# Optimization experiments

Hardware: AMD Instinct MI355X
Metric: run time of the kernel (lower is better)

The kernel has to match this reference:

```python
import jax, jax.numpy as jnp
import numpy as np

VOCAB = 32000
D_MODEL = 192
N_LAYERS = 8
D_STATE = 64
EXPAND = 2
D_CONV = 3
NUM_CLASSES = 2
D_INNER = EXPAND * D_MODEL            # 384
DT_RANK = (D_MODEL + 15) // 16        # 12 (mamba_ssm default ceil(d_model/16))
EPS = 1e-6


def rmsnorm(x, w):
    return w * x * jax.lax.rsqrt(jnp.mean(x * x, axis=-1, keepdims=True) + EPS)


def selective_scan(u, dt, A, Bm, Cm):
    # u, dt: (b, T, d_inner); Bm, Cm: (b, T, d_state); A: (d_inner, d_state)
    def step(h, xs):
        dt_t, B_t, C_t, u_t = xs                      # (b,di),(b,ds),(b,ds),(b,di)
        dA = jnp.exp(dt_t[:, :, None] * A)            # (b, di, ds)
        h = dA * h + (dt_t * u_t)[:, :, None] * B_t[:, None, :]
        y = jnp.einsum('bdn,bn->bd', h, C_t)
        return h, y

    b = u.shape[0]
    h0 = jnp.zeros((b, D_INNER, D_STATE), u.dtype)
    xs = (jnp.swapaxes(dt, 0, 1), jnp.swapaxes(Bm, 0, 1),
          jnp.swapaxes(Cm, 0, 1), jnp.swapaxes(u, 0, 1))
    _, ys = jax.lax.scan(step, h0, xs)                # ys: (T, b, di)
    return jnp.swapaxes(ys, 0, 1)


def mamba_layer(x, p):
    # one residual Mamba block: x + Mamba(RMSNorm(x))
    norm_w, in_w, cw, cb, xpw, dtw, dtb, Alog, Dp, ow = p
    h = rmsnorm(x, norm_w)
    xz = jnp.einsum('btd,ed->bte', h, in_w)           # (b, T, 2*di)
    xi, z = jnp.split(xz, 2, axis=-1)
    # causal depthwise conv over time
    xc = jnp.swapaxes(xi, 1, 2)                       # (b, di, T)
    xc = jax.lax.conv_general_dilated(xc, cw[:, None, :], (1,),
                                      [(D_CONV - 1, 0)],
                                      feature_group_count=D_INNER)
    xi = jax.nn.silu(jnp.swapaxes(xc, 1, 2) + cb)
    dbl = jnp.einsum('btc,ec->bte', xi, xpw)          # (b, T, dt_rank+2*ds)
    dt_r = dbl[..., :DT_RANK]
    Bm = dbl[..., DT_RANK:DT_RANK + D_STATE]
    Cm = dbl[..., DT_RANK + D_STATE:]
    dt = jax.nn.softplus(jnp.einsum('btr,dr->btd', dt_r, dtw) + dtb)
    A = -jnp.exp(Alog)
    y = selective_scan(xi, dt, A, Bm, Cm) + xi * Dp
    y = y * jax.nn.silu(z)
    return x + jnp.einsum('bte,de->btd', y, ow)


def setup_inputs():
    key = jax.random.key(0)
    ks = jax.random.split(key, 12)
    B, L = 8, 1024
    s = 0.02
    input_ids = jax.random.randint(ks[0], (B, L), 0, VOCAB, dtype=jnp.int32)
    attention_mask = jnp.ones((B, L), dtype=jnp.int32)
    embed = jax.random.normal(ks[1], (VOCAB, D_MODEL), jnp.float32) * s
    cls = jax.random.normal(ks[2], (1, 1, D_MODEL), jnp.float32) * s
    norm_w = jnp.ones((N_LAYERS, D_MODEL), jnp.float32)
    in_proj_w = jax.random.normal(ks[3], (N_LAYERS, 2 * D_INNER, D_MODEL), jnp.float32) * s
    conv_w = jax.random.normal(ks[4], (N_LAYERS, D_INNER, D_CONV), jnp.float32) * s
    conv_b = jnp.zeros((N_LAYERS, D_INNER), jnp.float32)
    x_proj_w = jax.random.normal(ks[5], (N_LAYERS, DT_RANK + 2 * D_STATE, D_INNER), jnp.float32) * s
    dt_proj_w = jax.random.normal(ks[6], (N_LAYERS, D_INNER, DT_RANK), jnp.float32) * s
    dt_proj_b = jnp.zeros((N_LAYERS, D_INNER), jnp.float32)
    # mamba_ssm S4D-real init: A_log = log(1..d_state)
    A_log = jnp.log(jnp.tile(jnp.arange(1.0, D_STATE + 1, dtype=jnp.float32)[None, None, :],
                             (N_LAYERS, D_INNER, 1)))
    D_param = jnp.ones((N_LAYERS, D_INNER), jnp.float32)
    out_proj_w = jax.random.normal(ks[7], (N_LAYERS, D_MODEL, D_INNER), jnp.float32) * s
    final_norm_w = jnp.ones((D_MODEL,), jnp.float32)
    head_w = embed[:NUM_CLASSES]            # tie_embeddings=True
    head_b = jnp.zeros((NUM_CLASSES,), jnp.float32)
    return dict(input_ids=input_ids, attention_mask=attention_mask, embed=embed,
                cls=cls, norm_w=norm_w, in_proj_w=in_proj_w, conv_w=conv_w,
                conv_b=conv_b, x_proj_w=x_proj_w, dt_proj_w=dt_proj_w,
                dt_proj_b=dt_proj_b, A_log=A_log, D_param=D_param,
                out_proj_w=out_proj_w, final_norm_w=final_norm_w,
                head_w=head_w, head_b=head_b)


def reference(input_ids, attention_mask, embed, cls, norm_w, in_proj_w, conv_w,
              conv_b, x_proj_w, dt_proj_w, dt_proj_b, A_log, D_param,
              out_proj_w, final_norm_w, head_w, head_b):
    x = embed[input_ids]                               # (b, L, d)
    b = x.shape[0]
    x = jnp.concatenate([x, jnp.broadcast_to(cls, (b, 1, D_MODEL))], axis=1)
    layer_fn = jax.checkpoint(mamba_layer)

    def body(x, p):
        return layer_fn(x, p), None

    x, _ = jax.lax.scan(body, x, (norm_w, in_proj_w, conv_w, conv_b, x_proj_w,
                                  dt_proj_w, dt_proj_b, A_log, D_param, out_proj_w))
    x = rmsnorm(x, final_norm_w)
    m = attention_mask.astype(x.dtype)                 # (b, L)
    denom = jnp.clip(jnp.sum(m, axis=1, keepdims=True), 1.0, None)
    pooled = jnp.sum(x[:, :-1] * m[..., None], axis=1) / denom
    return pooled @ head_w.T + head_b                  # (b, num_classes)
```

## Files before the change

kernel.cpp:

```cpp
#include <hip/hip_runtime.h>
#include <hip/hip_bf16.h>
#include <cstddef>

namespace {

constexpr int NB   = 8;
constexpr int LSEQ = 1025;
constexpr int TSEQ = 1024;
constexpr int DM   = 192;
constexpr int DI   = 384;
constexpr int DXZ  = 768;
constexpr int DBLW = 140;
constexpr int DTR  = 12;
constexpr int NST  = 64;
constexpr int MROWS = NB * LSEQ;
constexpr int NCH  = 32;
constexpr int CS   = 32;
constexpr int NCH1 = NCH - 1;
constexpr int NDG  = DI / 64;
constexpr int HST  = 32;
constexpr int XPAD = 144;
constexpr float LOG2E = 1.4426950408889634f;

using bf16x8 = __attribute__((ext_vector_type(8))) short;
using f32x4  = __attribute__((ext_vector_type(4))) float;

__device__ __forceinline__ float waveReduceSum(float v) {
#pragma unroll
  for (int o = 32; o; o >>= 1) v += __shfl_xor(v, o, 64);
  return v;
}

__device__ __forceinline__ unsigned short f2bf(float v) {
  __hip_bfloat16 b = __float2bfloat16(v);
  return *reinterpret_cast<unsigned short*>(&b);
}
__device__ __forceinline__ float bf2f(unsigned short u) {
  return __uint_as_float(((unsigned)u) << 16);
}
__device__ __forceinline__ unsigned addpair_bf(unsigned a, unsigned b) {
  float alo = __uint_as_float(a << 16), ahi = __uint_as_float(a & 0xffff0000u);
  float blo = __uint_as_float(b << 16), bhi = __uint_as_float(b & 0xffff0000u);
  return ((unsigned)f2bf(alo + blo)) | (((unsigned)f2bf(ahi + bhi)) << 16);
}

__global__ void embed_kernel(const int* __restrict__ ids, const float* __restrict__ emb,
                             const float* __restrict__ cls, float* __restrict__ x) {
  int idx = blockIdx.x * blockDim.x + threadIdx.x;
  if (idx >= NB * LSEQ * DM) return;
  int d = idx % DM;
  int bt = idx / DM;
  int t = bt % LSEQ, b = bt / LSEQ;
  float v;
  if (t < TSEQ) v = emb[(size_t)ids[b * TSEQ + t] * DM + d];
  else          v = cls[d];
  x[idx] = v;
}

__global__ void cvt_bf16_kernel(const float* __restrict__ src, unsigned short* __restrict__ dst,
                                int n) {
  int idx = blockIdx.x * blockDim.x + threadIdx.x;
  if (idx < n) dst[idx] = f2bf(src[idx]);
}

__global__ void pad_xp_kernel(const float* __restrict__ src, unsigned short* __restrict__ dst) {
  int idx = blockIdx.x * blockDim.x + threadIdx.x;
  if (idx >= 8 * XPAD * DI) return;
  int k = idx % DI;
  int n = (idx / DI) % XPAD;
  int l = idx / (DI * XPAD);
  float v = (n < DBLW) ? src[((size_t)l * DBLW + n) * DI + k] : 0.f;
  dst[idx] = f2bf(v);
}

__global__ void transpose_batched(const float* __restrict__ in, float* __restrict__ out,
                                  int rows, int cols) {
  __shared__ float tile[32][33];
  int l = blockIdx.z;
  int r0 = blockIdx.y * 32, c0 = blockIdx.x * 32;
  const float* src = in + (size_t)l * rows * cols;
  float* dst = out + (size_t)l * rows * cols;
  int tx = threadIdx.x, ty = threadIdx.y;
#pragma unroll
  for (int i = 0; i < 32; i += 8) {
    int r = r0 + ty + i, c = c0 + tx;
    if (r < rows && c < cols) tile[ty + i][tx] = src[(size_t)r * cols + c];
  }
  __syncthreads();
#pragma unroll
  for (int i = 0; i < 32; i += 8) {
    int c = c0 + ty + i, r = r0 + tx;
    if (c < cols && r < rows) dst[(size_t)c * rows + r] = tile[tx][ty + i];
  }
}

__global__ __launch_bounds__(192)
void rmsnorm_kernel(const float* __restrict__ x, const float* __restrict__ w,
                    unsigned short* __restrict__ h) {
  int row = blockIdx.x;
  int d = threadIdx.x;
  float v = x[(size_t)row * DM + d];
  float ss = waveReduceSum(v * v);
  __shared__ float red[3];
  if ((d & 63) == 0) red[d >> 6] = ss;
  __syncthreads();
  float ms = (red[0] + red[1] + red[2]) * (1.f / DM);
  h[(size_t)row * DM + d] = f2bf(v * rsqrtf(ms + 1e-6f) * w[d]);
}

template <int EPI, int ASRC>
__global__ __launch_bounds__(256)
void gemm_mfma(const unsigned short* __restrict__ A, const unsigned short* __restrict__ Ab0,
               const unsigned short* __restrict__ Ab1, const unsigned short* __restrict__ W,
               float* __restrict__ C, unsigned short* __restrict__ Cb,
               int M, int Nw, int Nstore, int K, int ldc) {
  __shared__ unsigned short Alds[128][40];
  __shared__ unsigned short Wlds[64][40];
  const int tid = threadIdx.x;
  const int w = tid >> 6, lane = tid & 63;
  const int r16 = lane & 15, g = lane >> 4;
  const int row0 = blockIdx.y * 128, col0 = blockIdx.x * 64;

  f32x4 acc[2][4];
#pragma unroll
  for (int mi = 0; mi < 2; ++mi)
#pragma unroll
    for (int ni = 0; ni < 4; ++ni) acc[mi][ni] = (f32x4){0.f, 0.f, 0.f, 0.f};

  for (int k0 = 0; k0 < K; k0 += 32) {
#pragma unroll
    for (int cc = 0; cc < 2; ++cc) {
      int c = tid + cc * 256;
      int r = c >> 2, q = c & 3;
      uint4 v = make_uint4(0, 0, 0, 0);
      int grow = row0 + r;
      if (grow < M) {
        if (ASRC == 0) {
          v = *(const uint4*)(A + (size_t)grow * K + k0 + q * 8);
        } else {
          uint4 a = *(const uint4*)(Ab0 + (size_t)grow * K + k0 + q * 8);
          uint4 b = *(const uint4*)(Ab1 + (size_t)grow * K + k0 + q * 8);
          v.x = addpair_bf(a.x, b.x);
          v.y = addpair_bf(a.y, b.y);
          v.z = addpair_bf(a.z, b.z);
          v.w = addpair_bf(a.w, b.w);
        }
      }
      *(uint4*)&Alds[r][q * 8] = v;
    }
    {
      int r = tid >> 2, q = tid & 3;
      uint4 v = make_uint4(0, 0, 0, 0);
      int gn = col0 + r;
      if (gn < Nw) v = *(const uint4*)(W + (size_t)gn * K + k0 + q * 8);
      *(uint4*)&Wlds[r][q * 8] = v;
    }
    __syncthreads();
    bf16x8 a_f[2], b_f[4];
#pragma unroll
    for (int mi = 0; mi < 2; ++mi)
      a_f[mi] = *(const bf16x8*)&Alds[w * 32 + mi * 16 + r16][g * 8];
#pragma unroll
    for (int ni = 0; ni < 4; ++ni)
      b_f[ni] = *(const bf16x8*)&Wlds[ni * 16 + r16][g * 8];
#pragma unroll
    for (int mi = 0; mi < 2; ++mi)
#pragma unroll
      for (int ni = 0; ni < 4; ++ni)
        acc[mi][ni] = __builtin_amdgcn_mfma_f32_16x16x32_bf16(a_f[mi], b_f[ni],
                                                              acc[mi][ni], 0, 0, 0);
    __syncthreads();
  }
#pragma unroll
  for (int mi = 0; mi < 2; ++mi) {
#pragma unroll
    for (int reg = 0; reg < 4; ++reg) {
      int row = row0 + w * 32 + mi * 16 + g * 4 + reg;
      if (row >= M) continue;
#pragma unroll
      for (int ni = 0; ni < 4; ++ni) {
        int col = col0 + ni * 16 + r16;
        if (col >= Nstore) continue;
        size_t idx = (size_t)row * ldc + col;
        if (EPI == 1)      C[idx] += acc[mi][ni][reg];
        else if (EPI == 0) C[idx] = acc[mi][ni][reg];
        else               Cb[idx] = f2bf(acc[mi][ni][reg]);
      }
    }
  }
}

__global__ void conv_kernel(const unsigned short* __restrict__ xz16, const float* __restrict__ cw,
                            const float* __restrict__ cb, float* __restrict__ xi,
                            unsigned short* __restrict__ xi16, float* __restrict__ zg) {
  int idx = blockIdx.x * blockDim.x + threadIdx.x;
  if (idx >= NB * LSEQ * DI) return;
  int c = idx % DI;
  int bt = idx / DI;
  int t = bt % LSEQ, b = bt / LSEQ;
  const unsigned short* src = xz16 + (size_t)b * LSEQ * DXZ + c;
  float s = cb[c];
  float w0 = cw[c * 3 + 0], w1 = cw[c * 3 + 1], w2 = cw[c * 3 + 2];
  if (t >= 2) s = fmaf(w0, bf2f(src[(size_t)(t - 2) * DXZ]), s);
  if (t >= 1) s = fmaf(w1, bf2f(src[(size_t)(t - 1) * DXZ]), s);
  s = fmaf(w2, bf2f(src[(size_t)t * DXZ]), s);
  float sig = 1.f / (1.f + __expf(-s));
  float u = s * sig;
  xi[idx] = u;
  xi16[idx] = f2bf(u);
  float zv = bf2f(src[(size_t)t * DXZ + DI]);
  float zsig = 1.f / (1.f + __expf(-zv));
  zg[idx] = zv * zsig;
}

__global__ __launch_bounds__(384)
void dt_kernel(const float* __restrict__ dbl, const float* __restrict__ dtwT,
               const float* __restrict__ dtb, float* __restrict__ dtout) {
  int row0 = blockIdx.x * 4;
  int d = threadIdx.x;
  __shared__ float rr[4][DTR];
  if (d < 4 * DTR) rr[d / DTR][d % DTR] = dbl[(size_t)(row0 + d / DTR) * DBLW + (d % DTR)];
  float w[DTR];
#pragma unroll
  for (int r = 0; r < DTR; ++r) w[r] = dtwT[r * DI + d];
  float bias = dtb[d];
  __syncthreads();
#pragma unroll
  for (int q = 0; q < 4; ++q) {
    float s = bias;
#pragma unroll
    for (int r = 0; r < DTR; ++r) s = fmaf(rr[q][r], w[r], s);
    float sp = fmaxf(s, 0.f) + log1pf(__expf(-fabsf(s)));
    dtout[(size_t)(row0 + q) * DI + d] = sp;
  }
}


__global__ __launch_bounds__(768, 3)
void scan_pass1(const float* __restrict__ dtp_, const float* __restrict__ xi,
                const float* __restrict__ dbl, const float* __restrict__ Alog,
                float* __restrict__ cumdt, float* __restrict__ H) {
  __shared__ float Bt[CS][64];
  const int tid = threadIdx.x;
  const int w = tid >> 6, lane = tid & 63;
  const int dgrp = w >> 1, half = w & 1;
  const int b = blockIdx.x / NCH1;
  const int c = blockIdx.x % NCH1;
  const int bg = b * NDG + dgrp;
  const int d = dgrp * 64 + lane;
  const int n0 = half * HST;
  const int t0 = c * CS;

  {
    const float* srcB = dbl + ((size_t)b * LSEQ + t0) * DBLW + DTR + lane;
    for (int r = w; r < CS; r += 12) Bt[r][lane] = srcB[(size_t)r * DBLW];
  }

  const float* Ap = Alog + (size_t)d * NST;
  float a0 = __expf(Ap[0]);
  bool okl = true;
#pragma unroll
  for (int j = 0; j < HST; ++j) {
    float aj = __expf(Ap[n0 + j]);
    okl = okl && (fabsf(aj - (float)(n0 + j + 1) * a0) <= 1e-3f * (float)(n0 + j + 1) * fabsf(a0));
  }
  const bool fast = __all(okl);
  const float al2u = -a0 * LOG2E;

  float h[HST];
#pragma unroll
  for (int j = 0; j < HST; ++j) h[j] = 0.f;

  __syncthreads();

  const float* dtp = dtp_ + ((size_t)b * LSEQ + t0) * DI + d;
  const float* up  = xi   + ((size_t)b * LSEQ + t0) * DI + d;
  float cum = 0.f;
  float dtv = *dtp, uv = *up;

  if (fast) {
    for (int t = 0; t < CS; ++t) {
      float n_dt = 0.f, n_u = 0.f;
      if (t + 1 < CS) {
        dtp += DI; up += DI;
        n_dt = *dtp; n_u = *up;
      }
      float dtu = dtv * uv;
      float m = dtv * al2u;
      float r1 = exp2f(m);
      float p = (n0 == 0) ? r1 : exp2f(m * (float)(n0 + 1));
      float r2 = r1 * r1, r4 = r2 * r2;
      float s0 = p, s1 = p * r1, s2 = p * r2, s3 = s2 * r1;
#pragma unroll
      for (int k = 0; k < 8; ++k) {
        float4 B4 = *(const float4*)&Bt[t][n0 + 4 * k];
        h[4 * k + 0] = fmaf(s0, h[4 * k + 0], dtu * B4.x);
        h[4 * k + 1] = fmaf(s1, h[4 * k + 1], dtu * B4.y);
        h[4 * k + 2] = fmaf(s2, h[4 * k + 2], dtu * B4.z);
        h[4 * k + 3] = fmaf(s3, h[4 * k + 3], dtu * B4.w);
        if (k < 7) { s0 *= r4; s1 *= r4; s2 *= r4; s3 *= r4; }
      }
      cum += dtv;
      dtv = n_dt; uv = n_u;
    }
  } else {
    for (int t = 0; t < CS; ++t) {
      float n_dt = 0.f, n_u = 0.f;
      if (t + 1 < CS) {
        dtp += DI; up += DI;
        n_dt = *dtp; n_u = *up;
      }
      float dtu = dtv * uv;
      for (int j = 0; j < HST; ++j) {
        float aj = -__expf(Ap[n0 + j]) * LOG2E;
        h[j] = fmaf(exp2f(dtv * aj), h[j], dtu * Bt[t][n0 + j]);
      }
      cum += dtv;
      dtv = n_dt; uv = n_u;
    }
  }

  if (half == 0)
    cumdt[(size_t)bg * NCH1 * 64 + (size_t)c * 64 + lane] = cum;
  float* hp = H + ((size_t)bg * NCH + (c + 1)) * NST * 64 + (size_t)n0 * 64 + lane;
#pragma unroll
  for (int j = 0; j < HST; ++j) hp[j * 64] = h[j];
}

__global__ __launch_bounds__(256)
void scan_pass2(const float* __restrict__ cumdt, const float* __restrict__ Alog,
                float* __restrict__ H) {
  int gw = blockIdx.x * 4 + (threadIdx.x >> 6);
  int lane = threadIdx.x & 63;
  int bg = gw >> 4;
  int nq = (gw & 15) * 4;
  int dgrp = bg % NDG;
  int d = dgrp * 64 + lane;

  float al2[4];
#pragma unroll
  for (int j = 0; j < 4; ++j) al2[j] = -__expf(Alog[(size_t)d * NST + nq + j]) * LOG2E;

  float h[4] = {0.f, 0.f, 0.f, 0.f};

  float* H0 = H + ((size_t)bg * NCH) * NST * 64 + (size_t)nq * 64 + lane;
#pragma unroll
  for (int j = 0; j < 4; ++j) H0[j * 64] = 0.f;

  for (int c = 1; c < NCH; ++c) {
    float cum = cumdt[(size_t)bg * NCH1 * 64 + (size_t)(c - 1) * 64 + lane];
    float* Hc = H + ((size_t)bg * NCH + c) * NST * 64 + (size_t)nq * 64 + lane;
#pragma unroll
    for (int j = 0; j < 4; ++j) {
      float he = Hc[j * 64];
      h[j] = fmaf(exp2f(al2[j] * cum), h[j], he);
      Hc[j * 64] = h[j];
    }
  }
}

__global__ __launch_bounds__(768, 3)
void scan_pass3(const float* __restrict__ dtp_, const float* __restrict__ xi,
                const float* __restrict__ zg, const float* __restrict__ dbl,
                const float* __restrict__ Alog, const float* __restrict__ Dpar,
                const float* __restrict__ H, unsigned short* __restrict__ yb0,
                unsigned short* __restrict__ yb1) {
  __shared__ float Bt[CS + 1][64];
  __shared__ float Ct[CS + 1][64];
  const int tid = threadIdx.x;
  const int w = tid >> 6, lane = tid & 63;
  const int dgrp = w >> 1, half = w & 1;
  const int b = blockIdx.x >> 5;
  const int c = blockIdx.x & 31;
  const int bg = b * NDG + dgrp;
  const int d = dgrp * 64 + lane;
  const int n0 = half * HST;
  const int t0 = c * CS;
  const int nsteps = (c == NCH - 1) ? (LSEQ - t0) : CS;

  {
    if (w < 6) {
      const float* srcB = dbl + ((size_t)b * LSEQ + t0) * DBLW + DTR + lane;
      for (int r = w; r < nsteps; r += 6) Bt[r][lane] = srcB[(size_t)r * DBLW];
    } else {
      const float* srcC = dbl + ((size_t)b * LSEQ + t0) * DBLW + DTR + NST + lane;
      for (int r = w - 6; r < nsteps; r += 6) Ct[r][lane] = srcC[(size_t)r * DBLW];
    }
  }

  const float* Ap = Alog + (size_t)d * NST;
  float a0 = __expf(Ap[0]);
  bool okl = true;
#pragma unroll
  for (int j = 0; j < HST; ++j) {
    float aj = __expf(Ap[n0 + j]);
    okl = okl && (fabsf(aj - (float)(n0 + j + 1) * a0) <= 1e-3f * (float)(n0 + j + 1) * fabsf(a0));
  }
  const bool fast = __all(okl);
  const float al2u = -a0 * LOG2E;

  float Dp = Dpar[d];
  float h[HST];
  {
    const float* hi = H + ((size_t)bg * NCH + c) * NST * 64 + (size_t)n0 * 64 + lane;
#pragma unroll
    for (int j = 0; j < HST; ++j) h[j] = hi[j * 64];
  }

  __syncthreads();

  const float* dtp = dtp_ + ((size_t)b * LSEQ + t0) * DI + d;
  const float* up  = xi   + ((size_t)b * LSEQ + t0) * DI + d;
  const float* gp  = zg   + ((size_t)b * LSEQ + t0) * DI + d;
  unsigned short* yp = (half == 0 ? yb0 : yb1) + ((size_t)b * LSEQ + t0) * DI + d;

  float dtv = *dtp, uv = *up, gv = *gp;

  if (fast) {
    for (int t = 0; t < nsteps; ++t) {
      float n_dt = 0.f, n_u = 0.f, n_g = 0.f;
      if (t + 1 < nsteps) {
        dtp += DI; up += DI; gp += DI;
        n_dt = *dtp; n_u = *up; n_g = *gp;
      }
      float dtu = dtv * uv;
      float m = dtv * al2u;
      float r1 = exp2f(m);
      float p = (n0 == 0) ? r1 : exp2f(m * (float)(n0 + 1));
      float r2 = r1 * r1, r4 = r2 * r2;
      float s0 = p, s1 = p * r1, s2 = p * r2, s3 = s2 * r1;
      float y = 0.f;
#pragma unroll
      for (int k = 0; k < 8; ++k) {
        float4 B4 = *(const float4*)&Bt[t][n0 + 4 * k];
        float4 C4 = *(const float4*)&Ct[t][n0 + 4 * k];
        h[4 * k + 0] = fmaf(s0, h[4 * k + 0], dtu * B4.x);
        y = fmaf(h[4 * k + 0], C4.x, y);
        h[4 * k + 1] = fmaf(s1, h[4 * k + 1], dtu * B4.y);
        y = fmaf(h[4 * k + 1], C4.y, y);
        h[4 * k + 2] = fmaf(s2, h[4 * k + 2], dtu * B4.z);
        y = fmaf(h[4 * k + 2], C4.z, y);
        h[4 * k + 3] = fmaf(s3, h[4 * k + 3], dtu * B4.w);
        y = fmaf(h[4 * k + 3], C4.w, y);
        if (k < 7) { s0 *= r4; s1 *= r4; s2 *= r4; s3 *= r4; }
      }
      float outv = (half == 0) ? fmaf(uv, Dp, y) * gv : y * gv;
      *yp = f2bf(outv);
      yp += DI;
      dtv = n_dt; uv = n_u; gv = n_g;
    }
  } else {
    for (int t = 0; t < nsteps; ++t) {
      float n_dt = 0.f, n_u = 0.f, n_g = 0.f;
      if (t + 1 < nsteps) {
        dtp += DI; up += DI; gp += DI;
        n_dt = *dtp; n_u = *up; n_g = *gp;
      }
      float dtu = dtv * uv;
      float y = 0.f;
      for (int j = 0; j < HST; ++j) {
        float aj = -__expf(Ap[n0 + j]) * LOG2E;
        h[j] = fmaf(exp2f(dtv * aj), h[j], dtu * Bt[t][n0 + j]);
        y = fmaf(h[j], Ct[t][n0 + j], y);
      }
      float outv = (half == 0) ? fmaf(uv, Dp, y) * gv : y * gv;
      *yp = f2bf(outv);
      yp += DI;
      dtv = n_dt; uv = n_u; gv = n_g;
    }
  }
}

__global__ __launch_bounds__(192)
void pool1_kernel(const float* __restrict__ x, const int* __restrict__ mask,
                  const float* __restrict__ fw, float* __restrict__ partial) {
  int b = blockIdx.x >> 6;
  int chunk = blockIdx.x & 63;
  int d = threadIdx.x;
  __shared__ float red[3];
  float w = fw[d];
  float acc = 0.f;
  for (int tt = 0; tt < 16; ++tt) {
    int t = chunk * 16 + tt;
    float v = x[((size_t)b * LSEQ + t) * DM + d];
    float ss = waveReduceSum(v * v);
    if ((d & 63) == 0) red[d >> 6] = ss;
    __syncthreads();
    float ms = (red[0] + red[1] + red[2]) * (1.f / DM);
    float m = (float)mask[b * TSEQ + t];
    acc = fmaf(v * rsqrtf(ms + 1e-6f) * w, m, acc);
    __syncthreads();
  }
  partial[((size_t)b * 64 + chunk) * DM + d] = acc;
}

__global__ __launch_bounds__(192)
void pool2_kernel(const float* __restrict__ partial, const int* __restrict__ mask,
                  const float* __restrict__ hw, const float* __restrict__ hb,
                  float* __restrict__ out) {
  int b = blockIdx.x;
  int d = threadIdx.x;
  float s = 0.f;
  for (int c = 0; c < 64; ++c) s += partial[((size_t)b * 64 + c) * DM + d];
  float den = 0.f;
  for (int t = d; t < TSEQ; t += DM) den += (float)mask[b * TSEQ + t];
  den = waveReduceSum(den);
  __shared__ float dred[3];
  __shared__ float pooled[DM];
  if ((d & 63) == 0) dred[d >> 6] = den;
  __syncthreads();
  float denom = fmaxf(dred[0] + dred[1] + dred[2], 1.f);
  pooled[d] = s / denom;
  __syncthreads();
  if (d < 2) {
    float acc = hb[d];
    for (int k = 0; k < DM; ++k) acc = fmaf(pooled[k], hw[d * DM + k], acc);
    out[b * 2 + d] = acc;
  }
}

}

extern "C" void kernel_launch(void* const* d_in, const int* in_sizes, int n_in,
                              void* d_out, int out_size, void* d_ws, size_t ws_size,
                              hipStream_t stream) {
  const int*   ids    = (const int*)d_in[0];
  const int*   mask   = (const int*)d_in[1];
  const float* embed  = (const float*)d_in[2];
  const float* cls    = (const float*)d_in[3];
  const float* norm_w = (const float*)d_in[4];
  const float* in_w   = (const float*)d_in[5];
  const float* conv_w = (const float*)d_in[6];
  const float* conv_b = (const float*)d_in[7];
  const float* xp_w   = (const float*)d_in[8];
  const float* dtw    = (const float*)d_in[9];
  const float* dtb    = (const float*)d_in[10];
  const float* Alog   = (const float*)d_in[11];
  const float* Dpar   = (const float*)d_in[12];
  const float* ow     = (const float*)d_in[13];
  const float* fnw    = (const float*)d_in[14];
  const float* hw     = (const float*)d_in[15];
  const float* hb     = (const float*)d_in[16];
  float* out = (float*)d_out;

  char* base = (char*)d_ws;
  size_t off = 0;
  auto alloc = [&](size_t bytes) -> void* {
    void* p = base + off;
    off = (off + bytes + 255) & ~(size_t)255;
    return p;
  };

  float* x      = (float*)alloc((size_t)NB * LSEQ * DM * 4);
  unsigned short* h16 = (unsigned short*)alloc((size_t)NB * LSEQ * DM * 2);
  unsigned short* xz16 = (unsigned short*)alloc((size_t)NB * LSEQ * DXZ * 2);
  float* xi     = (float*)alloc((size_t)NB * LSEQ * DI * 4);
  unsigned short* xi16 = (unsigned short*)alloc((size_t)NB * LSEQ * DI * 2);
  float* zgbuf  = (float*)alloc((size_t)NB * LSEQ * DI * 4);
  float* dblb   = (float*)alloc((size_t)NB * LSEQ * DBLW * 4);
  float* dtbuf  = (float*)alloc((size_t)NB * LSEQ * DI * 4);
  unsigned short* yb0 = (unsigned short*)alloc((size_t)NB * LSEQ * DI * 2);
  unsigned short* yb1 = (unsigned short*)alloc((size_t)NB * LSEQ * DI * 2);
  unsigned short* wb_in = (unsigned short*)alloc((size_t)8 * DXZ * DM * 2);
  unsigned short* wb_xp = (unsigned short*)alloc((size_t)8 * XPAD * DI * 2);
  unsigned short* wb_ow = (unsigned short*)alloc((size_t)8 * DM * DI * 2);
  float* wT_dt  = (float*)alloc((size_t)8 * DTR * DI * 4);
  float* partial = (float*)alloc((size_t)NB * 64 * DM * 4);
  float* cumdt  = (float*)alloc((size_t)NB * NDG * NCH1 * 64 * 4);
  float* Hbuf   = (float*)alloc((size_t)NB * NDG * NCH * NST * 64 * 4);

  cvt_bf16_kernel<<<(8 * DXZ * DM + 255) / 256, 256, 0, stream>>>(in_w, wb_in, 8 * DXZ * DM);
  pad_xp_kernel<<<(8 * XPAD * DI + 255) / 256, 256, 0, stream>>>(xp_w, wb_xp);
  cvt_bf16_kernel<<<(8 * DM * DI + 255) / 256, 256, 0, stream>>>(ow, wb_ow, 8 * DM * DI);
  dim3 tb(32, 8);
  transpose_batched<<<dim3(1, 12, 8), tb, 0, stream>>>(dtw, wT_dt, DI, DTR);

  embed_kernel<<<(NB * LSEQ * DM) / 256, 256, 0, stream>>>(ids, embed, cls, x);

  const int mtiles = (MROWS + 127) / 128;
  for (int l = 0; l < 8; ++l) {
    rmsnorm_kernel<<<MROWS, 192, 0, stream>>>(x, norm_w + l * DM, h16);
    gemm_mfma<2, 0><<<dim3(DXZ / 64, mtiles), 256, 0, stream>>>(
        h16, nullptr, nullptr, wb_in + (size_t)l * DXZ * DM, nullptr, xz16,
        MROWS, DXZ, DXZ, DM, DXZ);
    conv_kernel<<<(NB * LSEQ * DI) / 256, 256, 0, stream>>>(
        xz16, conv_w + l * DI * 3, conv_b + l * DI, xi, xi16, zgbuf);
    gemm_mfma<0, 0><<<dim3(XPAD / 64 + 1, mtiles), 256, 0, stream>>>(
        xi16, nullptr, nullptr, wb_xp + (size_t)l * XPAD * DI, dblb, nullptr,
        MROWS, XPAD, DBLW, DI, DBLW);
    dt_kernel<<<MROWS / 4, DI, 0, stream>>>(dblb, wT_dt + l * DTR * DI, dtb + l * DI, dtbuf);
    scan_pass1<<<NB * NCH1, 768, 0, stream>>>(
        dtbuf, xi, dblb, Alog + (size_t)l * DI * NST, cumdt, Hbuf);
    scan_pass2<<<(NB * NDG * 16) / 4, 256, 0, stream>>>(
        cumdt, Alog + (size_t)l * DI * NST, Hbuf);
    scan_pass3<<<NB * NCH, 768, 0, stream>>>(
        dtbuf, xi, zgbuf, dblb, Alog + (size_t)l * DI * NST, Dpar + l * DI, Hbuf,
        yb0, yb1);
    gemm_mfma<1, 1><<<dim3(DM / 64, mtiles), 256, 0, stream>>>(
        nullptr, yb0, yb1, wb_ow + (size_t)l * DM * DI, x, nullptr,
        MROWS, DM, DM, DI, DM);
  }

  pool1_kernel<<<NB * 64, 192, 0, stream>>>(x, mask, fnw, partial);
  pool2_kernel<<<NB, 192, 0, stream>>>(partial, mask, hw, hb, out);
}
```

Baseline: 1.261 ms.

## Store conv outputs as bf16 and halve scan chunk size for more blocks

The conv kernel now writes only bf16 copies of the activated input and gated z. The scan passes read these bf16 buffers instead of fp32 ones, which removes two fp32 intermediate buffers and cuts memory traffic. The chunked scan goes from 32 chunks of 32 steps to 64 chunks of 16 steps, doubling the block count and raising the launch-bounds occupancy hint for better parallelism. This costs precision in u and the gate, and makes the sequential cross-chunk pass2 twice as long and the H buffer twice as large.

```diff
diff --git a/kernel.cpp b/kernel.cpp
--- a/kernel.cpp
+++ b/kernel.cpp
@@ -14,8 +14,8 @@
 constexpr int DTR  = 12;
 constexpr int NST  = 64;
 constexpr int MROWS = NB * LSEQ;
-constexpr int NCH  = 32;
-constexpr int CS   = 32;
+constexpr int NCH  = 64;
+constexpr int CS   = 16;
 constexpr int NCH1 = NCH - 1;
 constexpr int NDG  = DI / 64;
 constexpr int HST  = 32;
@@ -191,8 +191,9 @@
 }
 
 __global__ void conv_kernel(const unsigned short* __restrict__ xz16, const float* __restrict__ cw,
-                            const float* __restrict__ cb, float* __restrict__ xi,
-                            unsigned short* __restrict__ xi16, float* __restrict__ zg) {
+                            const float* __restrict__ cb,
+                            unsigned short* __restrict__ xi16,
+                            unsigned short* __restrict__ zg16) {
   int idx = blockIdx.x * blockDim.x + threadIdx.x;
   if (idx >= NB * LSEQ * DI) return;
   int c = idx % DI;
@@ -206,11 +207,10 @@
   s = fmaf(w2, bf2f(src[(size_t)t * DXZ]), s);
   float sig = 1.f / (1.f + __expf(-s));
   float u = s * sig;
-  xi[idx] = u;
   xi16[idx] = f2bf(u);
   float zv = bf2f(src[(size_t)t * DXZ + DI]);
   float zsig = 1.f / (1.f + __expf(-zv));
-  zg[idx] = zv * zsig;
+  zg16[idx] = f2bf(zv * zsig);
 }
 
 __global__ __launch_bounds__(384)
@@ -236,8 +236,8 @@
 }
 
 
-__global__ __launch_bounds__(768, 3)
-void scan_pass1(const float* __restrict__ dtp_, const float* __restrict__ xi,
+__global__ __launch_bounds__(768, 6)
+void scan_pass1(const float* __restrict__ dtp_, const unsigned short* __restrict__ xi16,
                 const float* __restrict__ dbl, const float* __restrict__ Alog,
                 float* __restrict__ cumdt, float* __restrict__ H) {
   __shared__ float Bt[CS][64];
@@ -274,16 +274,16 @@
   __syncthreads();
 
   const float* dtp = dtp_ + ((size_t)b * LSEQ + t0) * DI + d;
-  const float* up  = xi   + ((size_t)b * LSEQ + t0) * DI + d;
+  const unsigned short* up = xi16 + ((size_t)b * LSEQ + t0) * DI + d;
   float cum = 0.f;
-  float dtv = *dtp, uv = *up;
+  float dtv = *dtp, uv = bf2f(*up);
 
   if (fast) {
     for (int t = 0; t < CS; ++t) {
       float n_dt = 0.f, n_u = 0.f;
       if (t + 1 < CS) {
         dtp += DI; up += DI;
-        n_dt = *dtp; n_u = *up;
+        n_dt = *dtp; n_u = bf2f(*up);
       }
       float dtu = dtv * uv;
       float m = dtv * al2u;
@@ -308,7 +308,7 @@
       float n_dt = 0.f, n_u = 0.f;
       if (t + 1 < CS) {
         dtp += DI; up += DI;
-        n_dt = *dtp; n_u = *up;
+        n_dt = *dtp; n_u = bf2f(*up);
       }
       float dtu = dtv * uv;
       for (int j = 0; j < HST; ++j) {
@@ -359,9 +359,9 @@
   }
 }
 
-__global__ __launch_bounds__(768, 3)
-void scan_pass3(const float* __restrict__ dtp_, const float* __restrict__ xi,
-                const float* __restrict__ zg, const float* __restrict__ dbl,
+__global__ __launch_bounds__(768, 6)
+void scan_pass3(const float* __restrict__ dtp_, const unsigned short* __restrict__ xi16,
+                const unsigned short* __restrict__ zg16, const float* __restrict__ dbl,
                 const float* __restrict__ Alog, const float* __restrict__ Dpar,
                 const float* __restrict__ H, unsigned short* __restrict__ yb0,
                 unsigned short* __restrict__ yb1) {
@@ -370,8 +370,8 @@
   const int tid = threadIdx.x;
   const int w = tid >> 6, lane = tid & 63;
   const int dgrp = w >> 1, half = w & 1;
-  const int b = blockIdx.x >> 5;
-  const int c = blockIdx.x & 31;
+  const int b = blockIdx.x >> 6;
+  const int c = blockIdx.x & 63;
   const int bg = b * NDG + dgrp;
   const int d = dgrp * 64 + lane;
   const int n0 = half * HST;
@@ -410,18 +410,18 @@
   __syncthreads();
 
   const float* dtp = dtp_ + ((size_t)b * LSEQ + t0) * DI + d;
-  const float* up  = xi   + ((size_t)b * LSEQ + t0) * DI + d;
-  const float* gp  = zg   + ((size_t)b * LSEQ + t0) * DI + d;
+  const unsigned short* up = xi16 + ((size_t)b * LSEQ + t0) * DI + d;
+  const unsigned short* gp = zg16 + ((size_t)b * LSEQ + t0) * DI + d;
   unsigned short* yp = (half == 0 ? yb0 : yb1) + ((size_t)b * LSEQ + t0) * DI + d;
 
-  float dtv = *dtp, uv = *up, gv = *gp;
+  float dtv = *dtp, uv = bf2f(*up), gv = bf2f(*gp);
 
   if (fast) {
     for (int t = 0; t < nsteps; ++t) {
       float n_dt = 0.f, n_u = 0.f, n_g = 0.f;
       if (t + 1 < nsteps) {
         dtp += DI; up += DI; gp += DI;
-        n_dt = *dtp; n_u = *up; n_g = *gp;
+        n_dt = *dtp; n_u = bf2f(*up); n_g = bf2f(*gp);
       }
       float dtu = dtv * uv;
       float m = dtv * al2u;
@@ -454,7 +454,7 @@
       float n_dt = 0.f, n_u = 0.f, n_g = 0.f;
       if (t + 1 < nsteps) {
         dtp += DI; up += DI; gp += DI;
-        n_dt = *dtp; n_u = *up; n_g = *gp;
+        n_dt = *dtp; n_u = bf2f(*up); n_g = bf2f(*gp);
       }
       float dtu = dtv * uv;
       float y = 0.f;
@@ -554,9 +554,8 @@
   float* x      = (float*)alloc((size_t)NB * LSEQ * DM * 4);
   unsigned short* h16 = (unsigned short*)alloc((size_t)NB * LSEQ * DM * 2);
   unsigned short* xz16 = (unsigned short*)alloc((size_t)NB * LSEQ * DXZ * 2);
-  float* xi     = (float*)alloc((size_t)NB * LSEQ * DI * 4);
   unsigned short* xi16 = (unsigned short*)alloc((size_t)NB * LSEQ * DI * 2);
-  float* zgbuf  = (float*)alloc((size_t)NB * LSEQ * DI * 4);
+  unsigned short* zg16 = (unsigned short*)alloc((size_t)NB * LSEQ * DI * 2);
   float* dblb   = (float*)alloc((size_t)NB * LSEQ * DBLW * 4);
   float* dtbuf  = (float*)alloc((size_t)NB * LSEQ * DI * 4);
   unsigned short* yb0 = (unsigned short*)alloc((size_t)NB * LSEQ * DI * 2);
@@ -584,17 +583,17 @@
         h16, nullptr, nullptr, wb_in + (size_t)l * DXZ * DM, nullptr, xz16,
         MROWS, DXZ, DXZ, DM, DXZ);
     conv_kernel<<<(NB * LSEQ * DI) / 256, 256, 0, stream>>>(
-        xz16, conv_w + l * DI * 3, conv_b + l * DI, xi, xi16, zgbuf);
+        xz16, conv_w + l * DI * 3, conv_b + l * DI, xi16, zg16);
     gemm_mfma<0, 0><<<dim3(XPAD / 64 + 1, mtiles), 256, 0, stream>>>(
         xi16, nullptr, nullptr, wb_xp + (size_t)l * XPAD * DI, dblb, nullptr,
         MROWS, XPAD, DBLW, DI, DBLW);
     dt_kernel<<<MROWS / 4, DI, 0, stream>>>(dblb, wT_dt + l * DTR * DI, dtb + l * DI, dtbuf);
     scan_pass1<<<NB * NCH1, 768, 0, stream>>>(
-        dtbuf, xi, dblb, Alog + (size_t)l * DI * NST, cumdt, Hbuf);
+        dtbuf, xi16, dblb, Alog + (size_t)l * DI * NST, cumdt, Hbuf);
     scan_pass2<<<(NB * NDG * 16) / 4, 256, 0, stream>>>(
         cumdt, Alog + (size_t)l * DI * NST, Hbuf);
     scan_pass3<<<NB * NCH, 768, 0, stream>>>(
-        dtbuf, xi, zgbuf, dblb, Alog + (size_t)l * DI * NST, Dpar + l * DI, Hbuf,
+        dtbuf, xi16, zg16, dblb, Alog + (size_t)l * DI * NST, Dpar + l * DI, Hbuf,
         yb0, yb1);
     gemm_mfma<1, 1><<<dim3(DM / 64, mtiles), 256, 0, stream>>>(
         nullptr, yb0, yb1, wb_ow + (size_t)l * DM * DI, x, nullptr,
```

After: 1.391 ms. 1.1x slower.
